# Optimization experiments

Hardware: AMD Instinct MI355X
Metric: run time of the kernel (lower is better)

## Reference

```python
import jax, jax.numpy as jnp
import numpy as np

N, P, D, H = 4, 2048, 512, 8
HD = D // H  # 64


def setup_inputs() -> dict:
    key = jax.random.key(0)
    ks = jax.random.split(key, 5)
    s = 1.0 / np.sqrt(HD)
    return {
        "xyz": jax.random.normal(ks[0], (N, P, D), dtype=jnp.float32),
        "Wq": jax.random.normal(ks[1], (HD, HD), dtype=jnp.float32) * s,
        "Wk": jax.random.normal(ks[2], (HD, HD), dtype=jnp.float32) * s,
        "Wv": jax.random.normal(ks[3], (HD, HD), dtype=jnp.float32) * s,
        "Wo": jax.random.normal(ks[4], (D, D), dtype=jnp.float32) * (1.0 / np.sqrt(D)),
        "bo": jnp.zeros((D,), dtype=jnp.float32),
    }


def reference(xyz, Wq, Wk, Wv, Wo, bo):
    n, p, d = xyz.shape
    x = xyz.reshape(n, p, H, HD)                      # (n, p, h, hd)
    # torch Linear: y = x @ W^T (shared per-head projection)
    q = jnp.einsum('nphd,ed->nphe', x, Wq)
    k = jnp.einsum('nphd,ed->nphe', x, Wk)
    v = jnp.einsum('nphd,ed->nphe', x, Wv)
    scale = 1.0 / jnp.sqrt(jnp.float32(d))            # source divides by sqrt(point_features_dim)
    energy = jnp.einsum('nqhd,nkhd->nhqk', q, k) * scale
    attention = jax.nn.softmax(energy, axis=-1)       # (n, h, q, k)
    out = jnp.einsum('nhqk,nkhd->nqhd', attention, v).reshape(n, p, d)
    out = jnp.einsum('npd,ed->npe', out, Wo) + bo
    return out, attention
```

## Files before the change

kernel.cpp:

```cpp
#include <hip/hip_runtime.h>

#define N_ 4
#define P_ 2048
#define D_ 512
#define H_ 8
#define HD_ 64

typedef __attribute__((ext_vector_type(8))) short short8;
typedef __attribute__((ext_vector_type(4))) float f32x4;

__device__ __forceinline__ f32x4 mfma16(short8 a, short8 b, f32x4 c){
  return __builtin_amdgcn_mfma_f32_16x16x32_bf16(a, b, c, 0, 0, 0);
}

__device__ __forceinline__ unsigned short f2bf(float f){
  union { float fv; unsigned u; } v; v.fv = f;
  unsigned r = v.u + 0x7fffu + ((v.u >> 16) & 1u);
  return (unsigned short)(r >> 16);
}
__device__ __forceinline__ float bf2f(unsigned short b){
  union { unsigned u; float fv; } v; v.u = ((unsigned)b) << 16;
  return v.fv;
}
__device__ __forceinline__ short8 load8f_bf(const float* p){
  f32x4 a = *(const f32x4*)p;
  f32x4 b = *(const f32x4*)(p + 4);
  short8 v;
  v[0]=(short)f2bf(a[0]); v[1]=(short)f2bf(a[1]); v[2]=(short)f2bf(a[2]); v[3]=(short)f2bf(a[3]);
  v[4]=(short)f2bf(b[0]); v[5]=(short)f2bf(b[1]); v[6]=(short)f2bf(b[2]); v[7]=(short)f2bf(b[3]);
  return v;
}

__global__ __launch_bounds__(256) void cast_wo_kernel(
    const float* __restrict__ Wo, unsigned short* __restrict__ Wob){
  int i = blockIdx.x * 256 + threadIdx.x;
  Wob[i] = f2bf(Wo[i]);
}

__global__ __launch_bounds__(256) void qkv_kernel(
    const float* __restrict__ x, const float* __restrict__ Wq,
    const float* __restrict__ Wk, const float* __restrict__ Wv,
    unsigned short* __restrict__ Q, unsigned short* __restrict__ K,
    unsigned short* __restrict__ Vt)
{
  const int n = blockIdx.z, h = blockIdx.y, pt = blockIdx.x;
  const int tid = threadIdx.x;
  const int wave = tid >> 6, lane = tid & 63, quad = lane >> 4, ln = lane & 15;
  const int p0 = pt * 64 + wave * 16;

  const float* xp = x + ((size_t)(n * P_ + p0 + ln)) * D_ + h * HD_ + quad * 8;
  short8 af0 = load8f_bf(xp);
  short8 af1 = load8f_bf(xp + 32);

  const size_t slab = ((size_t)(n * H_ + h)) * (size_t)P_ * HD_;
  const float* Ws[3] = {Wq, Wk, Wv};
  #pragma unroll
  for (int mat = 0; mat < 3; mat++){
    const float* W = Ws[mat];
    #pragma unroll
    for (int et = 0; et < 4; et++){
      const float* wp = W + (et * 16 + ln) * HD_ + quad * 8;
      short8 b0 = load8f_bf(wp);
      short8 b1 = load8f_bf(wp + 32);
      f32x4 c = {0.f, 0.f, 0.f, 0.f};
      c = mfma16(af0, b0, c);
      c = mfma16(af1, b1, c);
      #pragma unroll
      for (int r = 0; r < 4; r++){
        unsigned short v = f2bf(c[r]);
        int prow = p0 + quad * 4 + r;
        if (mat == 0)      Q [slab + (size_t)prow * HD_ + et * 16 + ln] = v;
        else if (mat == 1) K [slab + (size_t)prow * HD_ + et * 16 + ln] = v;
        else               Vt[slab + (size_t)(et * 16 + ln) * P_ + prow] = v;
      }
    }
  }
}

__global__ __launch_bounds__(256) void attn_kernel(
    const unsigned short* __restrict__ Q, const unsigned short* __restrict__ K,
    const unsigned short* __restrict__ Vt, float* __restrict__ attn,
    unsigned short* __restrict__ O1)
{
  __shared__ __align__(16) unsigned short ptile[4][16 * 40];
  const int n = blockIdx.z, h = blockIdx.y, qt = blockIdx.x;
  const int tid = threadIdx.x;
  const int wave = tid >> 6, lane = tid & 63, quad = lane >> 4, ln = lane & 15;
  const int q0 = qt * 64 + wave * 16;
  const float scale = 0.04419417382415922f;

  const size_t slab = ((size_t)(n * H_ + h)) * (size_t)P_ * HD_;
  const unsigned short* Qs = Q + slab;
  const unsigned short* Ks = K + slab;
  const unsigned short* Vs = Vt + slab;

  short8 qf0 = *(const short8*)(Qs + (size_t)(q0 + ln) * HD_ + quad * 8);
  short8 qf1 = *(const short8*)(Qs + (size_t)(q0 + ln) * HD_ + quad * 8 + 32);

  f32x4 l = {0.f, 0.f, 0.f, 0.f};
  for (int kt = 0; kt < P_ / 16; kt++){
    const unsigned short* kp = Ks + (size_t)(kt * 16 + ln) * HD_ + quad * 8;
    short8 kf0 = *(const short8*)kp;
    short8 kf1 = *(const short8*)(kp + 32);
    f32x4 s = {0.f, 0.f, 0.f, 0.f};
    s = mfma16(qf0, kf0, s);
    s = mfma16(qf1, kf1, s);
    #pragma unroll
    for (int r = 0; r < 4; r++) l[r] += __expf(s[r] * scale);
  }
  #pragma unroll
  for (int m = 1; m < 16; m <<= 1){
    #pragma unroll
    for (int r = 0; r < 4; r++) l[r] += __shfl_xor(l[r], m, 64);
  }
  f32x4 rinv;
  #pragma unroll
  for (int r = 0; r < 4; r++) rinv[r] = 1.0f / l[r];

  f32x4 o[4] = {{0,0,0,0},{0,0,0,0},{0,0,0,0},{0,0,0,0}};
  unsigned short* pl = ptile[wave];
  float* arow = attn + ((size_t)((n * H_ + h) * P_ + q0 + ln)) * P_;
  for (int kg = 0; kg < P_ / 32; kg++){
    #pragma unroll
    for (int t = 0; t < 2; t++){
      int kt = kg * 2 + t;
      const unsigned short* kp = Ks + (size_t)(kt * 16 + ln) * HD_ + quad * 8;
      short8 kf0 = *(const short8*)kp;
      short8 kf1 = *(const short8*)(kp + 32);
      f32x4 s = {0.f, 0.f, 0.f, 0.f};
      s = mfma16(qf0, kf0, s);
      s = mfma16(qf1, kf1, s);
      #pragma unroll
      for (int r = 0; r < 4; r++){
        float p = __expf(s[r] * scale) * rinv[r];
        pl[(quad * 4 + r) * 40 + t * 16 + ln] = f2bf(p);
      }
    }
    asm volatile("s_waitcnt lgkmcnt(0)" ::: "memory");
    short8 pf = *(const short8*)(pl + ln * 40 + quad * 8);
    f32x4 pa, pb;
    #pragma unroll
    for (int j = 0; j < 4; j++) pa[j] = bf2f((unsigned short)pf[j]);
    #pragma unroll
    for (int j = 0; j < 4; j++) pb[j] = bf2f((unsigned short)pf[4 + j]);
    float* ap = arow + kg * 32 + quad * 8;
    *(f32x4*)ap = pa;
    *(f32x4*)(ap + 4) = pb;
    #pragma unroll
    for (int dt = 0; dt < 4; dt++){
      short8 vf = *(const short8*)(Vs + (size_t)(dt * 16 + ln) * P_ + kg * 32 + quad * 8);
      o[dt] = mfma16(pf, vf, o[dt]);
    }
  }
  #pragma unroll
  for (int dt = 0; dt < 4; dt++){
    #pragma unroll
    for (int r = 0; r < 4; r++){
      int prow = q0 + quad * 4 + r;
      O1[((size_t)(n * P_ + prow)) * D_ + h * HD_ + dt * 16 + ln] = f2bf(o[dt][r]);
    }
  }
}

__global__ __launch_bounds__(256) void oproj_kernel(
    const unsigned short* __restrict__ O1, const unsigned short* __restrict__ Wob,
    const float* __restrict__ bo, float* __restrict__ out)
{
  const int mb = blockIdx.x, nb = blockIdx.y;
  const int tid = threadIdx.x;
  const int wave = tid >> 6, lane = tid & 63, quad = lane >> 4, ln = lane & 15;
  const int row0 = mb * 64 + wave * 16;
  const int col0 = nb * 64;
  f32x4 acc[4] = {{0,0,0,0},{0,0,0,0},{0,0,0,0},{0,0,0,0}};
  for (int ks = 0; ks < D_ / 32; ks++){
    short8 af = *(const short8*)(O1 + (size_t)(row0 + ln) * D_ + ks * 32 + quad * 8);
    #pragma unroll
    for (int et = 0; et < 4; et++){
      short8 bf = *(const short8*)(Wob + (size_t)(col0 + et * 16 + ln) * D_ + ks * 32 + quad * 8);
      acc[et] = mfma16(af, bf, acc[et]);
    }
  }
  #pragma unroll
  for (int et = 0; et < 4; et++){
    float b = bo[col0 + et * 16 + ln];
    #pragma unroll
    for (int r = 0; r < 4; r++){
      out[(size_t)(row0 + quad * 4 + r) * D_ + col0 + et * 16 + ln] = acc[et][r] + b;
    }
  }
}

extern "C" void kernel_launch(void* const* d_in, const int* in_sizes, int n_in,
                              void* d_out, int out_size, void* d_ws, size_t ws_size,
                              hipStream_t stream)
{
  (void)in_sizes; (void)n_in; (void)out_size; (void)ws_size;
  const float* xyz = (const float*)d_in[0];
  const float* Wq  = (const float*)d_in[1];
  const float* Wk  = (const float*)d_in[2];
  const float* Wv  = (const float*)d_in[3];
  const float* Wo  = (const float*)d_in[4];
  const float* bo  = (const float*)d_in[5];

  float* out  = (float*)d_out;
  float* attn = out + (size_t)N_ * P_ * D_;

  unsigned char* ws = (unsigned char*)d_ws;
  unsigned short* Q   = (unsigned short*)(ws);
  unsigned short* K   = (unsigned short*)(ws + (size_t)8  * 1024 * 1024);
  unsigned short* Vt  = (unsigned short*)(ws + (size_t)16 * 1024 * 1024);
  unsigned short* O1  = (unsigned short*)(ws + (size_t)24 * 1024 * 1024);
  unsigned short* Wob = (unsigned short*)(ws + (size_t)32 * 1024 * 1024);

  hipLaunchKernelGGL(cast_wo_kernel, dim3((D_ * D_) / 256), dim3(256), 0, stream, Wo, Wob);
  hipLaunchKernelGGL(qkv_kernel, dim3(P_ / 64, H_, N_), dim3(256), 0, stream,
                     xyz, Wq, Wk, Wv, Q, K, Vt);
  hipLaunchKernelGGL(attn_kernel, dim3(P_ / 64, H_, N_), dim3(256), 0, stream,
                     Q, K, Vt, attn, O1);
  hipLaunchKernelGGL(oproj_kernel, dim3((N_ * P_) / 64, D_ / 64, 1), dim3(256), 0, stream,
                     O1, Wob, bo, out);
}
```

Before: 923.5 us.

## Split attention key range across wave pairs with LDS reduction of sums and outputs

Each block now handles 32 queries instead of 64, and two waves share each 16-query group, each covering half of the key range. Row sums are exchanged through shared memory, and the partial PV outputs are summed in LDS before the bf16 write. This doubles the grid and shortens each wave's serial loop. It also adds software prefetch of K in the row-sum pass, nontemporal stores for the attention matrix and a launch_bounds occupancy hint. The trade-off is two block-wide barriers and extra LDS use.

```diff
diff --git a/kernel.cpp b/kernel.cpp
--- a/kernel.cpp
+++ b/kernel.cpp
@@ -77,16 +77,19 @@
   }
 }
 
-__global__ __launch_bounds__(256) void attn_kernel(
+__global__ __launch_bounds__(256, 8) void attn_kernel(
     const unsigned short* __restrict__ Q, const unsigned short* __restrict__ K,
     const unsigned short* __restrict__ Vt, float* __restrict__ attn,
     unsigned short* __restrict__ O1)
 {
   __shared__ __align__(16) unsigned short ptile[4][16 * 40];
+  __shared__ float lsum[4][4][4];
+  __shared__ float osum[2][64][17];
   const int n = blockIdx.z, h = blockIdx.y, qt = blockIdx.x;
   const int tid = threadIdx.x;
   const int wave = tid >> 6, lane = tid & 63, quad = lane >> 4, ln = lane & 15;
-  const int q0 = qt * 64 + wave * 16;
+  const int g = wave >> 1, hf = wave & 1;
+  const int q0 = qt * 32 + g * 16;
   const float scale = 0.04419417382415922f;
 
   const size_t slab = ((size_t)(n * H_ + h)) * (size_t)P_ * HD_;
@@ -97,14 +100,20 @@
   short8 qf0 = *(const short8*)(Qs + (size_t)(q0 + ln) * HD_ + quad * 8);
   short8 qf1 = *(const short8*)(Qs + (size_t)(q0 + ln) * HD_ + quad * 8 + 32);
 
+  const unsigned short* kp0 = Ks + (size_t)(hf * (P_ / 2) + ln) * HD_ + quad * 8;
+  short8 kf0 = *(const short8*)kp0;
+  short8 kf1 = *(const short8*)(kp0 + 32);
   f32x4 l = {0.f, 0.f, 0.f, 0.f};
-  for (int kt = 0; kt < P_ / 16; kt++){
-    const unsigned short* kp = Ks + (size_t)(kt * 16 + ln) * HD_ + quad * 8;
-    short8 kf0 = *(const short8*)kp;
-    short8 kf1 = *(const short8*)(kp + 32);
+  for (int kt = 0; kt < P_ / 32; kt++){
+    short8 c0 = kf0, c1 = kf1;
+    if (kt < P_ / 32 - 1){
+      const unsigned short* np = kp0 + (size_t)(kt + 1) * 16 * HD_;
+      kf0 = *(const short8*)np;
+      kf1 = *(const short8*)(np + 32);
+    }
     f32x4 s = {0.f, 0.f, 0.f, 0.f};
-    s = mfma16(qf0, kf0, s);
-    s = mfma16(qf1, kf1, s);
+    s = mfma16(qf0, c0, s);
+    s = mfma16(qf1, c1, s);
     #pragma unroll
     for (int r = 0; r < 4; r++) l[r] += __expf(s[r] * scale);
   }
@@ -113,23 +122,30 @@
     #pragma unroll
     for (int r = 0; r < 4; r++) l[r] += __shfl_xor(l[r], m, 64);
   }
+  if (ln == 0){
+    #pragma unroll
+    for (int r = 0; r < 4; r++) lsum[wave][quad][r] = l[r];
+  }
+  __syncthreads();
   f32x4 rinv;
   #pragma unroll
-  for (int r = 0; r < 4; r++) rinv[r] = 1.0f / l[r];
+  for (int r = 0; r < 4; r++) rinv[r] = 1.0f / (l[r] + lsum[wave ^ 1][quad][r]);
 
   f32x4 o[4] = {{0,0,0,0},{0,0,0,0},{0,0,0,0},{0,0,0,0}};
   unsigned short* pl = ptile[wave];
   float* arow = attn + ((size_t)((n * H_ + h) * P_ + q0 + ln)) * P_;
-  for (int kg = 0; kg < P_ / 32; kg++){
+  const int kgbeg = hf * (P_ / 64);
+  for (int i = 0; i < P_ / 64; i++){
+    int kg = kgbeg + i;
     #pragma unroll
     for (int t = 0; t < 2; t++){
       int kt = kg * 2 + t;
       const unsigned short* kp = Ks + (size_t)(kt * 16 + ln) * HD_ + quad * 8;
-      short8 kf0 = *(const short8*)kp;
-      short8 kf1 = *(const short8*)(kp + 32);
+      short8 ka = *(const short8*)kp;
+      short8 kb = *(const short8*)(kp + 32);
       f32x4 s = {0.f, 0.f, 0.f, 0.f};
-      s = mfma16(qf0, kf0, s);
-      s = mfma16(qf1, kf1, s);
+      s = mfma16(qf0, ka, s);
+      s = mfma16(qf1, kb, s);
       #pragma unroll
       for (int r = 0; r < 4; r++){
         float p = __expf(s[r] * scale) * rinv[r];
@@ -144,20 +160,32 @@
     #pragma unroll
     for (int j = 0; j < 4; j++) pb[j] = bf2f((unsigned short)pf[4 + j]);
     float* ap = arow + kg * 32 + quad * 8;
-    *(f32x4*)ap = pa;
-    *(f32x4*)(ap + 4) = pb;
+    __builtin_nontemporal_store(pa, (f32x4*)ap);
+    __builtin_nontemporal_store(pb, (f32x4*)(ap + 4));
     #pragma unroll
     for (int dt = 0; dt < 4; dt++){
       short8 vf = *(const short8*)(Vs + (size_t)(dt * 16 + ln) * P_ + kg * 32 + quad * 8);
       o[dt] = mfma16(pf, vf, o[dt]);
     }
   }
-  #pragma unroll
-  for (int dt = 0; dt < 4; dt++){
-    #pragma unroll
-    for (int r = 0; r < 4; r++){
-      int prow = q0 + quad * 4 + r;
-      O1[((size_t)(n * P_ + prow)) * D_ + h * HD_ + dt * 16 + ln] = f2bf(o[dt][r]);
+
+  if (hf){
+    #pragma unroll
+    for (int dt = 0; dt < 4; dt++){
+      #pragma unroll
+      for (int r = 0; r < 4; r++) osum[g][lane][dt * 4 + r] = o[dt][r];
+    }
+  }
+  __syncthreads();
+  if (!hf){
+    #pragma unroll
+    for (int dt = 0; dt < 4; dt++){
+      #pragma unroll
+      for (int r = 0; r < 4; r++){
+        float val = o[dt][r] + osum[g][lane][dt * 4 + r];
+        int prow = q0 + quad * 4 + r;
+        O1[((size_t)(n * P_ + prow)) * D_ + h * HD_ + dt * 16 + ln] = f2bf(val);
+      }
     }
   }
 }
@@ -215,7 +243,7 @@
   hipLaunchKernelGGL(cast_wo_kernel, dim3((D_ * D_) / 256), dim3(256), 0, stream, Wo, Wob);
   hipLaunchKernelGGL(qkv_kernel, dim3(P_ / 64, H_, N_), dim3(256), 0, stream,
                      xyz, Wq, Wk, Wv, Q, K, Vt);
-  hipLaunchKernelGGL(attn_kernel, dim3(P_ / 64, H_, N_), dim3(256), 0, stream,
+  hipLaunchKernelGGL(attn_kernel, dim3(P_ / 32, H_, N_), dim3(256), 0, stream,
                      Q, K, Vt, attn, O1);
   hipLaunchKernelGGL(oproj_kernel, dim3((N_ * P_) / 64, D_ / 64, 1), dim3(256), 0, stream,
                      O1, Wob, bo, out);
```

After: 890.0 us. -3.6%, faster.
